# Kernel optimization log

Hardware: AMD Instinct MI355X
Metric: run time of the kernel (lower is better)

The kernel has to match this reference:

```python
import jax, jax.numpy as jnp
import numpy as np

DIM = 1024
H = 56
NS = 32            # n_state == head_v_dim
KEY_DIM = H * NS   # 1792
D_INNER = H * NS   # 1792
T_LEN = 2048
B = 4


def _xavier(key, fan_out, fan_in):
    bound = (6.0 / (fan_in + fan_out)) ** 0.5
    return jax.random.uniform(key, (fan_out, fan_in), jnp.float32, -bound, bound)


def setup_inputs() -> dict:
    key = jax.random.key(0)
    ks = jax.random.split(key, 8)
    x = jax.random.normal(ks[0], (T_LEN, B, DIM), jnp.float32)
    S = jnp.zeros((B, H, NS, NS), jnp.float32)
    Wq = _xavier(ks[1], KEY_DIM, DIM)
    Wk = _xavier(ks[2], KEY_DIM, DIM)
    Wv = _xavier(ks[3], D_INNER, DIM)
    Wa = _xavier(ks[4], H, DIM)
    Wout = _xavier(ks[5], DIM, D_INNER)
    A_log = jax.random.uniform(ks[6], (H,), jnp.float32, -5.0, -1.0)
    dt_bias = jax.random.uniform(ks[7], (H,), jnp.float32, 0.5, 1.5)
    return {"x": x, "S": S, "Wq": Wq, "Wk": Wk, "Wv": Wv, "Wa": Wa,
            "A_log": A_log, "dt_bias": dt_bias, "Wout": Wout}


def _l2norm(t):
    # matches F.normalize(dim=-1): x / max(||x||, 1e-12)
    n = jnp.sqrt(jnp.sum(t * t, axis=-1, keepdims=True))
    return t / jnp.maximum(n, 1e-12)


def reference(x, S, Wq, Wk, Wv, Wa, A_log, dt_bias, Wout):
    T, Bb, _ = x.shape
    q = jax.nn.silu(x @ Wq.T).reshape(T, Bb, H, NS)
    k = jax.nn.silu(x @ Wk.T).reshape(T, Bb, H, NS)
    v = jax.nn.silu(x @ Wv.T).reshape(T, Bb, H, NS)
    q = _l2norm(q)
    k = _l2norm(k)
    a = x @ Wa.T                                   # [T,B,H]
    dt = jax.nn.softplus(a + dt_bias)
    decay = jnp.exp(-jnp.exp(A_log) * dt)          # [T,B,H]

    def step(S_t, inp):
        k_t, v_t, q_t, d_t = inp                   # [B,H,NS], [B,H,NS], [B,H,NS], [B,H]
        retrieved = jnp.einsum('bhij,bhi->bhj', S_t, k_t)   # S^T k
        delta = v_t - retrieved
        outer = k_t[..., :, None] * delta[..., None, :]     # [B,H,NS,NS] = k ox delta
        S_t = S_t + jnp.tanh(d_t[..., None, None] * S_t + outer)
        Sq = jnp.einsum('bhij,bhi->bhj', S_t, q_t)
        return S_t, Sq

    S_new, out = jax.lax.scan(step, S, (k, v, q, decay))
    out = out.reshape(T, Bb, D_INNER) @ Wout.T     # [T,B,dim]
    return out, S_new
```

## Files before the change

kernel.cpp:

```cpp
#include <hip/hip_runtime.h>


typedef __attribute__((ext_vector_type(8))) __bf16 bf16x8;
typedef __attribute__((ext_vector_type(8))) _Float16 f16x8;
typedef __attribute__((ext_vector_type(4))) float f32x4;
typedef __attribute__((ext_vector_type(2))) float f32x2;

#define T_LEN 2048
#define BB 4
#define HH 56
#define NS 32
#define DIM 1024
#define KD 1792
#define MROWS 8192
#define CH 16
#define NCHUNK (T_LEN / CH)

#define VMCNT(N) asm volatile("s_waitcnt vmcnt(" #N ")" ::: "memory")
#define LGKM(N)  asm volatile("s_waitcnt lgkmcnt(" #N ")" ::: "memory")
#define SB       __builtin_amdgcn_sched_barrier(0)

__device__ __forceinline__ float bf2f(unsigned short u) {
    return __uint_as_float(((unsigned int)u) << 16);
}
__device__ __forceinline__ unsigned short f2bf(float f) {
    unsigned int u = __float_as_uint(f);
    u += 0x7fffu + ((u >> 16) & 1u);
    return (unsigned short)(u >> 16);
}
__device__ __forceinline__ unsigned short f2h(float f) {
    union { _Float16 h; unsigned short u; } cv;
    cv.h = (_Float16)f;
    return cv.u;
}
__device__ __forceinline__ float h2f(unsigned short u) {
    union { unsigned short u; _Float16 h; } cv;
    cv.u = u;
    return (float)cv.h;
}

__device__ __forceinline__ float tanh_fast(float x) {
    float e = __builtin_amdgcn_exp2f(x * 2.885390081777927f);
    float r = __builtin_amdgcn_rcpf(e + 1.0f);
    return fmaf(-2.0f, r, 1.0f);
}

__device__ __forceinline__ float dpp_sum16(float x) {
    int t;
    t = __builtin_amdgcn_update_dpp(0, __float_as_int(x), 0xB1, 0xf, 0xf, true);
    x += __int_as_float(t);
    t = __builtin_amdgcn_update_dpp(0, __float_as_int(x), 0x4E, 0xf, 0xf, true);
    x += __int_as_float(t);
    t = __builtin_amdgcn_update_dpp(0, __float_as_int(x), 0x141, 0xf, 0xf, true);
    x += __int_as_float(t);
    t = __builtin_amdgcn_update_dpp(0, __float_as_int(x), 0x140, 0xf, 0xf, true);
    x += __int_as_float(t);
    return x;
}

__device__ __forceinline__ f32x2 dpp_sum16x2(float a, float b) {
    int ta, tb;
    ta = __builtin_amdgcn_update_dpp(0, __float_as_int(a), 0xB1, 0xf, 0xf, true);
    tb = __builtin_amdgcn_update_dpp(0, __float_as_int(b), 0xB1, 0xf, 0xf, true);
    a += __int_as_float(ta); b += __int_as_float(tb);
    ta = __builtin_amdgcn_update_dpp(0, __float_as_int(a), 0x4E, 0xf, 0xf, true);
    tb = __builtin_amdgcn_update_dpp(0, __float_as_int(b), 0x4E, 0xf, 0xf, true);
    a += __int_as_float(ta); b += __int_as_float(tb);
    ta = __builtin_amdgcn_update_dpp(0, __float_as_int(a), 0x141, 0xf, 0xf, true);
    tb = __builtin_amdgcn_update_dpp(0, __float_as_int(b), 0x141, 0xf, 0xf, true);
    a += __int_as_float(ta); b += __int_as_float(tb);
    ta = __builtin_amdgcn_update_dpp(0, __float_as_int(a), 0x140, 0xf, 0xf, true);
    tb = __builtin_amdgcn_update_dpp(0, __float_as_int(b), 0x140, 0xf, 0xf, true);
    a += __int_as_float(ta); b += __int_as_float(tb);
    return (f32x2){a, b};
}

__device__ __forceinline__ void gload_lds16(const void* g, void* l) {
    __builtin_amdgcn_global_load_lds(
        (const __attribute__((address_space(1))) unsigned int*)g,
        (__attribute__((address_space(3))) unsigned int*)l, 16, 0, 0);
}
__device__ __forceinline__ void gload_lds4(const void* g, void* l) {
    __builtin_amdgcn_global_load_lds(
        (const __attribute__((address_space(1))) unsigned int*)g,
        (__attribute__((address_space(3))) unsigned int*)l, 4, 0, 0);
}

__device__ __forceinline__ unsigned lds_off(const void* p) {
    return (unsigned)(unsigned long long)
        (const __attribute__((address_space(3))) char*)p;
}

template <int OFF>
__device__ __forceinline__ f32x4 dsr128(unsigned a) {
    f32x4 r;
    asm volatile("ds_read_b128 %0, %1 offset:%2" : "=v"(r) : "v"(a), "n"(OFF));
    return r;
}
template <int OFF>
__device__ __forceinline__ f32x2 dsr64f(unsigned a) {
    f32x2 r;
    asm volatile("ds_read_b64 %0, %1 offset:%2" : "=v"(r) : "v"(a), "n"(OFF));
    return r;
}
template <int OFF>
__device__ __forceinline__ unsigned dsr32u(unsigned a) {
    unsigned r;
    asm volatile("ds_read_b32 %0, %1 offset:%2" : "=v"(r) : "v"(a), "n"(OFF));
    return r;
}
template <int OFF>
__device__ __forceinline__ float dsr32f(unsigned a) {
    float r;
    asm volatile("ds_read_b32 %0, %1 offset:%2" : "=v"(r) : "v"(a), "n"(OFF));
    return r;
}

__global__ void cast_split3_kernel(const float* __restrict__ in,
                                   unsigned short* __restrict__ hi,
                                   unsigned short* __restrict__ lo,
                                   unsigned short* __restrict__ h16, int n8) {
    int i = blockIdx.x * blockDim.x + threadIdx.x;
    if (i >= n8) return;
    const float4* p = (const float4*)in + (size_t)i * 2;
    float4 a = p[0], b = p[1];
    float xs[8] = {a.x, a.y, a.z, a.w, b.x, b.y, b.z, b.w};
    unsigned int ho[4], lv[4], hv[4];
#pragma unroll
    for (int c = 0; c < 4; ++c) {
        unsigned short h0 = f2bf(xs[2 * c]);
        unsigned short h1 = f2bf(xs[2 * c + 1]);
        unsigned short l0 = f2bf(xs[2 * c] - bf2f(h0));
        unsigned short l1 = f2bf(xs[2 * c + 1] - bf2f(h1));
        ho[c] = (unsigned int)h0 | ((unsigned int)h1 << 16);
        lv[c] = (unsigned int)l0 | ((unsigned int)l1 << 16);
        hv[c] = (unsigned int)f2h(xs[2 * c]) | ((unsigned int)f2h(xs[2 * c + 1]) << 16);
    }
    ((uint4*)hi)[i]  = (uint4){ho[0], ho[1], ho[2], ho[3]};
    ((uint4*)lo)[i]  = (uint4){lv[0], lv[1], lv[2], lv[3]};
    ((uint4*)h16)[i] = (uint4){hv[0], hv[1], hv[2], hv[3]};
}

__global__ void cast_split_kernel(const float* __restrict__ in,
                                  unsigned short* __restrict__ hi,
                                  unsigned short* __restrict__ lo, int n8) {
    int i = blockIdx.x * blockDim.x + threadIdx.x;
    if (i >= n8) return;
    const float4* p = (const float4*)in + (size_t)i * 2;
    float4 a = p[0], b = p[1];
    float xs[8] = {a.x, a.y, a.z, a.w, b.x, b.y, b.z, b.w};
    unsigned int ho[4], lv[4];
#pragma unroll
    for (int c = 0; c < 4; ++c) {
        unsigned short h0 = f2bf(xs[2 * c]);
        unsigned short h1 = f2bf(xs[2 * c + 1]);
        unsigned short l0 = f2bf(xs[2 * c] - bf2f(h0));
        unsigned short l1 = f2bf(xs[2 * c + 1] - bf2f(h1));
        ho[c] = (unsigned int)h0 | ((unsigned int)h1 << 16);
        lv[c] = (unsigned int)l0 | ((unsigned int)l1 << 16);
    }
    ((uint4*)hi)[i] = (uint4){ho[0], ho[1], ho[2], ho[3]};
    ((uint4*)lo)[i] = (uint4){lv[0], lv[1], lv[2], lv[3]};
}

__global__ void cast_half_kernel(const float* __restrict__ in,
                                 unsigned short* __restrict__ out, int n8) {
    int i = blockIdx.x * blockDim.x + threadIdx.x;
    if (i >= n8) return;
    const float4* p = (const float4*)in + (size_t)i * 2;
    float4 a = p[0], b = p[1];
    uint4 o;
    o.x = (unsigned int)f2h(a.x) | ((unsigned int)f2h(a.y) << 16);
    o.y = (unsigned int)f2h(a.z) | ((unsigned int)f2h(a.w) << 16);
    o.z = (unsigned int)f2h(b.x) | ((unsigned int)f2h(b.y) << 16);
    o.w = (unsigned int)f2h(b.z) | ((unsigned int)f2h(b.w) << 16);
    ((uint4*)out)[i] = o;
}

__device__ __forceinline__ void gemm_split(
    const unsigned short* __restrict__ Ah, const unsigned short* __restrict__ Al,
    const unsigned short* __restrict__ Bh, const unsigned short* __restrict__ Bl,
    int m0, int n0, int K, int bmax,
    unsigned short* AsH, unsigned short* AsL,
    unsigned short* BsH, unsigned short* BsL,
    f32x4 (&acc)[4][4]) {
    const int tid  = threadIdx.x;
    const int lane = tid & 63;
    const int wave = tid >> 6;
    const int wm = wave >> 1, wn = wave & 1;
    const int lr = lane & 15, lkb = lane >> 4;

#pragma unroll
    for (int fr = 0; fr < 4; ++fr)
#pragma unroll
        for (int fc = 0; fc < 4; ++fc) acc[fr][fc] = (f32x4){0.f, 0.f, 0.f, 0.f};

    auto stage = [&](int kt) {
#pragma unroll
        for (int c = 0; c < 2; ++c) {
            int i = c * 256 + tid;
            int r = i >> 2, kk = (i & 3) << 3;
            size_t ao = (size_t)(m0 + r) * K + kt + kk;
            int br = n0 + r; if (br > bmax) br = bmax;
            size_t bo = (size_t)br * K + kt + kk;
            gload_lds16(Ah + ao, AsH + i * 8);
            gload_lds16(Al + ao, AsL + i * 8);
            gload_lds16(Bh + bo, BsH + i * 8);
            gload_lds16(Bl + bo, BsL + i * 8);
        }
    };

    stage(0);
    const int nk = K >> 5;
    for (int t = 0; t < nk; ++t) {
        __syncthreads();
        bf16x8 ah[4], al[4], bh[4], bl[4];
#pragma unroll
        for (int f = 0; f < 4; ++f) {
            int ai = (wm * 64 + f * 16 + lr) * 32 + lkb * 8;
            int bi = (wn * 64 + f * 16 + lr) * 32 + lkb * 8;
            ah[f] = *(const bf16x8*)(AsH + ai);
            al[f] = *(const bf16x8*)(AsL + ai);
            bh[f] = *(const bf16x8*)(BsH + bi);
            bl[f] = *(const bf16x8*)(BsL + bi);
        }
#pragma unroll
        for (int fr = 0; fr < 4; ++fr)
#pragma unroll
            for (int fc = 0; fc < 4; ++fc) {
                acc[fr][fc] = __builtin_amdgcn_mfma_f32_16x16x32_bf16(
                    ah[fr], bh[fc], acc[fr][fc], 0, 0, 0);
                acc[fr][fc] = __builtin_amdgcn_mfma_f32_16x16x32_bf16(
                    ah[fr], bl[fc], acc[fr][fc], 0, 0, 0);
                acc[fr][fc] = __builtin_amdgcn_mfma_f32_16x16x32_bf16(
                    al[fr], bh[fc], acc[fr][fc], 0, 0, 0);
            }
        __syncthreads();
        if (t + 1 < nk) stage((t + 1) << 5);
    }
}

__global__ __launch_bounds__(256) void proj_split_kernel(
    const unsigned short* __restrict__ xh, const unsigned short* __restrict__ xl,
    const unsigned short* __restrict__ Wh, const unsigned short* __restrict__ Wl,
    const unsigned short* __restrict__ Wah, const unsigned short* __restrict__ Wal,
    const float* __restrict__ A_log, const float* __restrict__ dt_bias,
    float* __restrict__ dstF, float* __restrict__ decayb, int knorm) {
    __shared__ __align__(16) unsigned short AsH[128 * 32];
    __shared__ __align__(16) unsigned short AsL[128 * 32];
    __shared__ __align__(16) unsigned short BsH[128 * 32];
    __shared__ __align__(16) unsigned short BsL[128 * 32];

    const int tile = blockIdx.x;
    const bool isdecay = (tile == 14);
    int m0 = blockIdx.y * 128;
    int n0 = isdecay ? 0 : tile * 128;
    int bmax = isdecay ? (HH - 1) : (KD - 1);
    const unsigned short* Bh = isdecay ? Wah : Wh;
    const unsigned short* Bl = isdecay ? Wal : Wl;

    f32x4 acc[4][4];
    gemm_split(xh, xl, Bh, Bl, m0, n0, DIM, bmax, AsH, AsL, BsH, BsL, acc);

    const int lane = threadIdx.x & 63, wave = threadIdx.x >> 6;
    const int wm = wave >> 1, wn = wave & 1, lr = lane & 15, lkb = lane >> 4;

    if (isdecay) {
#pragma unroll
        for (int fr = 0; fr < 4; ++fr)
#pragma unroll
            for (int fc = 0; fc < 4; ++fc)
#pragma unroll
                for (int v = 0; v < 4; ++v) {
                    int m = m0 + wm * 64 + fr * 16 + lkb * 4 + v;
                    int n = n0 + wn * 64 + fc * 16 + lr;
                    int t = m >> 2, b = m & 3;
                    if (n < HH) {
                        float z = acc[fr][fc][v] + dt_bias[n];
                        float sp = (z > 20.f) ? z : log1pf(__expf(z));
                        decayb[((size_t)(b * HH + n)) * T_LEN + t] =
                            __expf(-__expf(A_log[n]) * sp);
                    }
                }
        return;
    }

    if (knorm) {
#pragma unroll
        for (int fr = 0; fr < 4; ++fr)
#pragma unroll
            for (int hc = 0; hc < 2; ++hc)
#pragma unroll
                for (int v = 0; v < 4; ++v) {
                    float yA = acc[fr][2 * hc][v];
                    float yB = acc[fr][2 * hc + 1][v];
                    float sA = yA / (1.f + __expf(-yA));
                    float sB = yB / (1.f + __expf(-yB));
                    float ss = fmaf(sA, sA, sB * sB);
                    ss = dpp_sum16(ss);
                    float sc = 1.f / fmaxf(sqrtf(ss), 1e-12f);
                    int m = m0 + wm * 64 + fr * 16 + lkb * 4 + v;
                    int t = m >> 2, b = m & 3;
                    int h = ((n0 + wn * 64) >> 5) + hc;
                    size_t ro = (((size_t)(b * HH + h)) * T_LEN + t) * NS;
                    dstF[ro + lr]      = sA * sc;
                    dstF[ro + lr + 16] = sB * sc;
                }
    } else {
#pragma unroll
        for (int fr = 0; fr < 4; ++fr)
#pragma unroll
            for (int fc = 0; fc < 4; ++fc)
#pragma unroll
                for (int v = 0; v < 4; ++v) {
                    int m = m0 + wm * 64 + fr * 16 + lkb * 4 + v;
                    int n = n0 + wn * 64 + fc * 16 + lr;
                    int t = m >> 2, b = m & 3;
                    int h = n >> 5, i = n & 31;
                    float y = acc[fr][fc][v];
                    float s = y / (1.f + __expf(-y));
                    dstF[(((size_t)(b * HH + h)) * T_LEN + t) * NS + i] = s;
                }
    }
}

__global__ __launch_bounds__(256) void q_gemm_f16_kernel(
    const unsigned short* __restrict__ xf, const unsigned short* __restrict__ Wqf,
    unsigned short* __restrict__ dstH) {
    __shared__ __align__(16) unsigned short As[128 * 32];
    __shared__ __align__(16) unsigned short Bs[128 * 32];
    int m0 = blockIdx.y * 128, n0 = blockIdx.x * 128;

    const int tid  = threadIdx.x;
    const int lane = tid & 63;
    const int wave = tid >> 6;
    const int wm = wave >> 1, wn = wave & 1;
    const int lr = lane & 15, lkb = lane >> 4;

    f32x4 acc[4][4];
#pragma unroll
    for (int fr = 0; fr < 4; ++fr)
#pragma unroll
        for (int fc = 0; fc < 4; ++fc) acc[fr][fc] = (f32x4){0.f, 0.f, 0.f, 0.f};

    auto stage = [&](int kt) {
#pragma unroll
        for (int c = 0; c < 2; ++c) {
            int i = c * 256 + tid;
            int r = i >> 2, kk = (i & 3) << 3;
            gload_lds16(xf + (size_t)(m0 + r) * DIM + kt + kk, As + i * 8);
            gload_lds16(Wqf + (size_t)(n0 + r) * DIM + kt + kk, Bs + i * 8);
        }
    };

    stage(0);
    const int nk = DIM >> 5;
    for (int t = 0; t < nk; ++t) {
        __syncthreads();
        f16x8 af[4], bf[4];
#pragma unroll
        for (int f = 0; f < 4; ++f) {
            af[f] = *(const f16x8*)(As + (wm * 64 + f * 16 + lr) * 32 + lkb * 8);
            bf[f] = *(const f16x8*)(Bs + (wn * 64 + f * 16 + lr) * 32 + lkb * 8);
        }
#pragma unroll
        for (int fr = 0; fr < 4; ++fr)
#pragma unroll
            for (int fc = 0; fc < 4; ++fc)
                acc[fr][fc] = __builtin_amdgcn_mfma_f32_16x16x32_f16(
                    af[fr], bf[fc], acc[fr][fc], 0, 0, 0);
        __syncthreads();
        if (t + 1 < nk) stage((t + 1) << 5);
    }

#pragma unroll
    for (int fr = 0; fr < 4; ++fr)
#pragma unroll
        for (int hc = 0; hc < 2; ++hc)
#pragma unroll
            for (int v = 0; v < 4; ++v) {
                float yA = acc[fr][2 * hc][v];
                float yB = acc[fr][2 * hc + 1][v];
                float sA = yA / (1.f + __expf(-yA));
                float sB = yB / (1.f + __expf(-yB));
                float ss = fmaf(sA, sA, sB * sB);
                ss = dpp_sum16(ss);
                float sc = 1.f / fmaxf(sqrtf(ss), 1e-12f);
                int m = m0 + wm * 64 + fr * 16 + lkb * 4 + v;
                int t = m >> 2, b = m & 3;
                int h = ((n0 + wn * 64) >> 5) + hc;
                size_t ro = (((size_t)(b * HH + h)) * T_LEN + t) * NS;
                dstH[ro + lr]      = f2h(sA * sc);
                dstH[ro + lr + 16] = f2h(sB * sc);
            }
}

__global__ __launch_bounds__(256) void out_gemm_kernel(
    const unsigned short* __restrict__ Sq, const unsigned short* __restrict__ Wo,
    float* __restrict__ out) {
    __shared__ __align__(16) unsigned short As[128 * 32];
    __shared__ __align__(16) unsigned short Bs[128 * 32];
    int m0 = blockIdx.y * 128, n0 = blockIdx.x * 128;

    const int tid  = threadIdx.x;
    const int lane = tid & 63;
    const int wave = tid >> 6;
    const int wm = wave >> 1, wn = wave & 1;
    const int lr = lane & 15, lkb = lane >> 4;

    f32x4 acc[4][4];
#pragma unroll
    for (int fr = 0; fr < 4; ++fr)
#pragma unroll
        for (int fc = 0; fc < 4; ++fc) acc[fr][fc] = (f32x4){0.f, 0.f, 0.f, 0.f};

    auto stage = [&](int kt) {
#pragma unroll
        for (int c = 0; c < 2; ++c) {
            int i = c * 256 + tid;
            int r = i >> 2, kk = (i & 3) << 3;
            gload_lds16(Sq + (size_t)(m0 + r) * KD + kt + kk, As + i * 8);
            gload_lds16(Wo + (size_t)(n0 + r) * KD + kt + kk, Bs + i * 8);
        }
    };

    stage(0);
    const int nk = KD >> 5;
    for (int t = 0; t < nk; ++t) {
        __syncthreads();
        f16x8 af[4], bf[4];
#pragma unroll
        for (int f = 0; f < 4; ++f) {
            af[f] = *(const f16x8*)(As + (wm * 64 + f * 16 + lr) * 32 + lkb * 8);
            bf[f] = *(const f16x8*)(Bs + (wn * 64 + f * 16 + lr) * 32 + lkb * 8);
        }
#pragma unroll
        for (int fr = 0; fr < 4; ++fr)
#pragma unroll
            for (int fc = 0; fc < 4; ++fc)
                acc[fr][fc] = __builtin_amdgcn_mfma_f32_16x16x32_f16(
                    af[fr], bf[fc], acc[fr][fc], 0, 0, 0);
        __syncthreads();
        if (t + 1 < nk) stage((t + 1) << 5);
    }

#pragma unroll
    for (int fr = 0; fr < 4; ++fr)
#pragma unroll
        for (int fc = 0; fc < 4; ++fc)
#pragma unroll
            for (int v = 0; v < 4; ++v) {
                int m = m0 + wm * 64 + fr * 16 + lkb * 4 + v;
                int n = n0 + wn * 64 + fc * 16 + lr;
                out[(size_t)m * DIM + n] = acc[fr][fc][v];
            }
}

__global__ __launch_bounds__(512, 1) void scan_kernel(
    const float* __restrict__ kf, const unsigned short* __restrict__ qh,
    const float* __restrict__ vf, const float* __restrict__ decayb,
    const float* __restrict__ S0, unsigned short* __restrict__ Sq,
    float* __restrict__ Sout) {
    __shared__ __align__(16) float          kbuf[4][CH][NS];
    __shared__ __align__(16) float          vbuf[4][CH][NS];
    __shared__ __align__(16) unsigned short qbuf[4][CH][NS];
    __shared__ __align__(16) float          dbuf[4][64];

    const int bh = blockIdx.x;
    const int b = bh / HH, h = bh - b * HH;
    const int tid = threadIdx.x;
    const int lane = tid & 63, wave = tid >> 6;
    const int col = tid >> 4;
    const int ii  = tid & 15;
    const int i0  = ii * 2;

    const float* Sp = S0 + (size_t)bh * NS * NS;
    float s0 = Sp[(i0 + 0) * NS + col];
    float s1 = Sp[(i0 + 1) * NS + col];

    const size_t base  = (size_t)bh * T_LEN * NS;
    const size_t dbase = (size_t)bh * T_LEN;
    const size_t cbcol = (size_t)h * NS;

    const unsigned kb0 = lds_off(&kbuf[0][0][0]) + (unsigned)i0 * 4;
    const unsigned qb0 = lds_off(&qbuf[0][0][0]) + (unsigned)i0 * 2;
    const unsigned vb0 = lds_off(&vbuf[0][0][0]) + (unsigned)col * 4;
    const unsigned db0 = lds_off(&dbuf[0][0]);

    auto stage = [&](int c) {
        int s = c & 3;
        if (wave == 0) {
            gload_lds16(kf + base + (size_t)c * 512 + lane * 4,
                        &kbuf[s][0][0] + lane * 4);
        } else if (wave == 1) {
            gload_lds16(kf + base + (size_t)c * 512 + 256 + lane * 4,
                        &kbuf[s][8][0] + lane * 4);
        } else if (wave == 2) {
            gload_lds16(vf + base + (size_t)c * 512 + lane * 4,
                        &vbuf[s][0][0] + lane * 4);
        } else if (wave == 3) {
            gload_lds16(vf + base + (size_t)c * 512 + 256 + lane * 4,
                        &vbuf[s][8][0] + lane * 4);
        } else if (wave == 4) {
            gload_lds16(qh + base + (size_t)c * 512 + lane * 8,
                        &qbuf[s][0][0] + lane * 8);
        } else if (wave == 5) {
            gload_lds4(decayb + dbase + (size_t)c * CH + lane,
                       &dbuf[s][0] + lane);
        }
    };

    stage(0);
    stage(1);
    VMCNT(0);
    __builtin_amdgcn_s_barrier();

    float o_pend = 0.f;

    for (int c = 0; c < NCHUNK; ++c) {
        if (c + 2 < NCHUNK) stage(c + 2);
        if (wave < 6) { VMCNT(18); }
        __builtin_amdgcn_s_barrier();
        SB;

        const int s = c & 3;
        const unsigned kb = kb0 + (unsigned)s * (CH * NS * 4);
        const unsigned qb = qb0 + (unsigned)s * (CH * NS * 2);
        const unsigned vb = vb0 + (unsigned)s * (CH * NS * 4);
        const unsigned db = db0 + (unsigned)s * 256;

        f32x2 kA[4], kB[4]; unsigned qA[4], qB[4]; float vA[4], vB[4];
        f32x4 dA, dB;

#define LDG(KK, QQ, VV, DV, g)                                          \
        KK[0] = dsr64f<((g) * 4 + 0) * 128>(kb);                        \
        KK[1] = dsr64f<((g) * 4 + 1) * 128>(kb);                        \
        KK[2] = dsr64f<((g) * 4 + 2) * 128>(kb);                        \
        KK[3] = dsr64f<((g) * 4 + 3) * 128>(kb);                        \
        QQ[0] = dsr32u<((g) * 4 + 0) * 64>(qb);                         \
        QQ[1] = dsr32u<((g) * 4 + 1) * 64>(qb);                         \
        QQ[2] = dsr32u<((g) * 4 + 2) * 64>(qb);                         \
        QQ[3] = dsr32u<((g) * 4 + 3) * 64>(qb);                         \
        VV[0] = dsr32f<((g) * 4 + 0) * 128>(vb);                        \
        VV[1] = dsr32f<((g) * 4 + 1) * 128>(vb);                        \
        VV[2] = dsr32f<((g) * 4 + 2) * 128>(vb);                        \
        VV[3] = dsr32f<((g) * 4 + 3) * 128>(vb);                        \
        DV    = dsr128<(g) * 16>(db);

#define CMP(KK, QQ, VV, DV, g)                                          \
        {                                                               \
            _Pragma("unroll")                                           \
            for (int p = 0; p < 4; ++p) {                               \
                const int t = c * CH + (g) * 4 + p;                     \
                float k0 = KK[p][0], k1 = KK[p][1];                     \
                float q0 = h2f((unsigned short)(QQ[p] & 0xffff));       \
                float q1 = h2f((unsigned short)(QQ[p] >> 16));          \
                float vj = VV[p];                                       \
                float d  = DV[p];                                       \
                float xr = fmaf(k1, s1, k0 * s0);                       \
                f32x2 rd = dpp_sum16x2(xr, o_pend);                     \
                if (ii == 0 && t > 0) {                                 \
                    size_t ro = ((size_t)(t - 1) * BB + b) * KD + cbcol;\
                    Sq[ro + col] = f2h(rd[1]);                          \
                }                                                       \
                float delta = vj - rd[0];                               \
                float a0 = fmaf(d, s0, k0 * delta);                     \
                float a1 = fmaf(d, s1, k1 * delta);                     \
                s0 += tanh_fast(a0); s1 += tanh_fast(a1);               \
                o_pend = fmaf(q1, s1, q0 * s0);                         \
            }                                                           \
        }

        LDG(kA, qA, vA, dA, 0);
        LDG(kB, qB, vB, dB, 1);
        LGKM(13); SB;
        CMP(kA, qA, vA, dA, 0);
        LDG(kA, qA, vA, dA, 2);
        LGKM(13); SB;
        CMP(kB, qB, vB, dB, 1);
        LDG(kB, qB, vB, dB, 3);
        LGKM(13); SB;
        CMP(kA, qA, vA, dA, 2);
        LGKM(0); SB;
        CMP(kB, qB, vB, dB, 3);
#undef LDG
#undef CMP
    }

    {
        float oo = dpp_sum16(o_pend);
        if (ii == 0) {
            size_t ro = ((size_t)(T_LEN - 1) * BB + b) * KD + cbcol;
            Sq[ro + col] = f2h(oo);
        }
    }

    float* so = Sout + (size_t)bh * NS * NS;
    so[(i0 + 0) * NS + col] = s0;
    so[(i0 + 1) * NS + col] = s1;
}

extern "C" void kernel_launch(void* const* d_in, const int* in_sizes, int n_in,
                              void* d_out, int out_size, void* d_ws, size_t ws_size,
                              hipStream_t stream) {
    const float* x       = (const float*)d_in[0];
    const float* S0      = (const float*)d_in[1];
    const float* Wq      = (const float*)d_in[2];
    const float* Wk      = (const float*)d_in[3];
    const float* Wv      = (const float*)d_in[4];
    const float* Wa      = (const float*)d_in[5];
    const float* A_log   = (const float*)d_in[6];
    const float* dt_bias = (const float*)d_in[7];
    const float* Wout    = (const float*)d_in[8];

    float* out  = (float*)d_out;
    float* Sout = out + (size_t)T_LEN * BB * DIM;

    char* w = (char*)d_ws;
    auto alloc = [&](size_t bytes) {
        char* p = w; w += (bytes + 255) & ~(size_t)255; return p;
    };
    unsigned short* xh  = (unsigned short*)alloc((size_t)MROWS * DIM * 2);
    unsigned short* xl  = (unsigned short*)alloc((size_t)MROWS * DIM * 2);
    unsigned short* Wbh = (unsigned short*)alloc((size_t)KD * DIM * 2);
    unsigned short* Wbl = (unsigned short*)alloc((size_t)KD * DIM * 2);
    unsigned short* Wah = (unsigned short*)alloc((size_t)HH * DIM * 2);
    unsigned short* Wal = (unsigned short*)alloc((size_t)HH * DIM * 2);
    float* kf           = (float*)alloc((size_t)MROWS * KD * 4);
    float* vf           = (float*)alloc((size_t)MROWS * KD * 4);
    unsigned short* Woh = (unsigned short*)alloc((size_t)DIM * KD * 2);
    unsigned short* Sq   = xh;
    unsigned short* xf16 = (unsigned short*)vf;

    unsigned short* qh  = (unsigned short*)d_out;
    float* decayb       = (float*)((char*)d_out + (size_t)MROWS * KD * 2);

    {
        int n8 = (int)((size_t)MROWS * DIM / 8);
        cast_split3_kernel<<<(n8 + 255) / 256, 256, 0, stream>>>(x, xh, xl, xf16, n8);
    }
    {
        int n8 = (int)((size_t)KD * DIM / 8);
        cast_half_kernel<<<(n8 + 255) / 256, 256, 0, stream>>>(Wq, Wbh, n8);
        q_gemm_f16_kernel<<<dim3(14, 64), 256, 0, stream>>>(xf16, Wbh, qh);
    }
    {
        int n8 = (int)((size_t)KD * DIM / 8);
        cast_split_kernel<<<(n8 + 255) / 256, 256, 0, stream>>>(Wk, Wbh, Wbl, n8);
        int n8a = (int)((size_t)HH * DIM / 8);
        cast_split_kernel<<<(n8a + 255) / 256, 256, 0, stream>>>(Wa, Wah, Wal, n8a);
        proj_split_kernel<<<dim3(15, 64), 256, 0, stream>>>(
            xh, xl, Wbh, Wbl, Wah, Wal, A_log, dt_bias, kf, decayb, 1);
    }
    {
        int n8 = (int)((size_t)KD * DIM / 8);
        cast_split_kernel<<<(n8 + 255) / 256, 256, 0, stream>>>(Wv, Wbh, Wbl, n8);
        proj_split_kernel<<<dim3(14, 64), 256, 0, stream>>>(
            xh, xl, Wbh, Wbl, Wah, Wal, A_log, dt_bias, vf, decayb, 0);
    }
    {
        int n8 = (int)((size_t)DIM * KD / 8);
        cast_half_kernel<<<(n8 + 255) / 256, 256, 0, stream>>>(Wout, Woh, n8);
    }
    scan_kernel<<<BB * HH, 512, 0, stream>>>(kf, qh, vf, decayb, S0, Sq, Sout);
    out_gemm_kernel<<<dim3(8, 64), 256, 0, stream>>>(Sq, Woh, out);
}
```

Baseline: 716.1 us.

## Fuse cast kernels, merge k/v projection launches, enlarge scan chunk with LDS-staged output

All fp32-to-bf16/fp16 weight and input casts now run in one kernel, which needs separate buffers for each weight. The k, v and decay projections are merged into one launch of 29 column tiles. The scan kernel doubles its chunk length to 32, unrolling more compute groups per barrier. It also buffers per-step outputs in LDS and has an idle wave write them out as coalesced 16-byte stores instead of scattered 2-byte stores. These changes cut launch count and tail effects and improve store coalescing, at the cost of more LDS and workspace plus retuned wait counts.

```diff
diff --git a/kernel.cpp b/kernel.cpp
--- a/kernel.cpp
+++ b/kernel.cpp
@@ -13,7 +13,7 @@
 #define DIM 1024
 #define KD 1792
 #define MROWS 8192
-#define CH 16
+#define CH 32
 #define NCHUNK (T_LEN / CH)
 
 #define VMCNT(N) asm volatile("s_waitcnt vmcnt(" #N ")" ::: "memory")
@@ -116,16 +116,12 @@
     return r;
 }
 
-__global__ void cast_split3_kernel(const float* __restrict__ in,
-                                   unsigned short* __restrict__ hi,
-                                   unsigned short* __restrict__ lo,
-                                   unsigned short* __restrict__ h16, int n8) {
-    int i = blockIdx.x * blockDim.x + threadIdx.x;
-    if (i >= n8) return;
+__device__ __forceinline__ void do_split8(const float* in, unsigned short* hi,
+                                          unsigned short* lo, int i) {
     const float4* p = (const float4*)in + (size_t)i * 2;
     float4 a = p[0], b = p[1];
     float xs[8] = {a.x, a.y, a.z, a.w, b.x, b.y, b.z, b.w};
-    unsigned int ho[4], lv[4], hv[4];
+    unsigned int ho[4], lv[4];
 #pragma unroll
     for (int c = 0; c < 4; ++c) {
         unsigned short h0 = f2bf(xs[2 * c]);
@@ -134,39 +130,11 @@
         unsigned short l1 = f2bf(xs[2 * c + 1] - bf2f(h1));
         ho[c] = (unsigned int)h0 | ((unsigned int)h1 << 16);
         lv[c] = (unsigned int)l0 | ((unsigned int)l1 << 16);
-        hv[c] = (unsigned int)f2h(xs[2 * c]) | ((unsigned int)f2h(xs[2 * c + 1]) << 16);
-    }
-    ((uint4*)hi)[i]  = (uint4){ho[0], ho[1], ho[2], ho[3]};
-    ((uint4*)lo)[i]  = (uint4){lv[0], lv[1], lv[2], lv[3]};
-    ((uint4*)h16)[i] = (uint4){hv[0], hv[1], hv[2], hv[3]};
-}
-
-__global__ void cast_split_kernel(const float* __restrict__ in,
-                                  unsigned short* __restrict__ hi,
-                                  unsigned short* __restrict__ lo, int n8) {
-    int i = blockIdx.x * blockDim.x + threadIdx.x;
-    if (i >= n8) return;
-    const float4* p = (const float4*)in + (size_t)i * 2;
-    float4 a = p[0], b = p[1];
-    float xs[8] = {a.x, a.y, a.z, a.w, b.x, b.y, b.z, b.w};
-    unsigned int ho[4], lv[4];
-#pragma unroll
-    for (int c = 0; c < 4; ++c) {
-        unsigned short h0 = f2bf(xs[2 * c]);
-        unsigned short h1 = f2bf(xs[2 * c + 1]);
-        unsigned short l0 = f2bf(xs[2 * c] - bf2f(h0));
-        unsigned short l1 = f2bf(xs[2 * c + 1] - bf2f(h1));
-        ho[c] = (unsigned int)h0 | ((unsigned int)h1 << 16);
-        lv[c] = (unsigned int)l0 | ((unsigned int)l1 << 16);
     }
     ((uint4*)hi)[i] = (uint4){ho[0], ho[1], ho[2], ho[3]};
     ((uint4*)lo)[i] = (uint4){lv[0], lv[1], lv[2], lv[3]};
 }
-
-__global__ void cast_half_kernel(const float* __restrict__ in,
-                                 unsigned short* __restrict__ out, int n8) {
-    int i = blockIdx.x * blockDim.x + threadIdx.x;
-    if (i >= n8) return;
+__device__ __forceinline__ void do_half8(const float* in, unsigned short* out, int i) {
     const float4* p = (const float4*)in + (size_t)i * 2;
     float4 a = p[0], b = p[1];
     uint4 o;
@@ -176,6 +144,55 @@
     o.w = (unsigned int)f2h(b.z) | ((unsigned int)f2h(b.w) << 16);
     ((uint4*)out)[i] = o;
 }
+
+__global__ void megacast_kernel(
+    const float* __restrict__ x, unsigned short* __restrict__ xh,
+    unsigned short* __restrict__ xl, unsigned short* __restrict__ xf16,
+    const float* __restrict__ Wk, unsigned short* __restrict__ Wkh,
+    unsigned short* __restrict__ Wkl,
+    const float* __restrict__ Wv, unsigned short* __restrict__ Wvh,
+    unsigned short* __restrict__ Wvl,
+    const float* __restrict__ Wa, unsigned short* __restrict__ Wah,
+    unsigned short* __restrict__ Wal,
+    const float* __restrict__ Wq, unsigned short* __restrict__ Wqh16,
+    const float* __restrict__ Wout, unsigned short* __restrict__ Woh) {
+    int i = blockIdx.x * blockDim.x + threadIdx.x;
+    const int N0 = MROWS * DIM / 8;
+    const int N1 = KD * DIM / 8;
+    const int N3 = HH * DIM / 8;
+    if (i < N0) {
+        const float4* p = (const float4*)x + (size_t)i * 2;
+        float4 a = p[0], b = p[1];
+        float xs[8] = {a.x, a.y, a.z, a.w, b.x, b.y, b.z, b.w};
+        unsigned int ho[4], lv[4], hv[4];
+#pragma unroll
+        for (int c = 0; c < 4; ++c) {
+            unsigned short h0 = f2bf(xs[2 * c]);
+            unsigned short h1 = f2bf(xs[2 * c + 1]);
+            unsigned short l0 = f2bf(xs[2 * c] - bf2f(h0));
+            unsigned short l1 = f2bf(xs[2 * c + 1] - bf2f(h1));
+            ho[c] = (unsigned int)h0 | ((unsigned int)h1 << 16);
+            lv[c] = (unsigned int)l0 | ((unsigned int)l1 << 16);
+            hv[c] = (unsigned int)f2h(xs[2 * c]) |
+                    ((unsigned int)f2h(xs[2 * c + 1]) << 16);
+        }
+        ((uint4*)xh)[i]   = (uint4){ho[0], ho[1], ho[2], ho[3]};
+        ((uint4*)xl)[i]   = (uint4){lv[0], lv[1], lv[2], lv[3]};
+        ((uint4*)xf16)[i] = (uint4){hv[0], hv[1], hv[2], hv[3]};
+        return;
+    }
+    i -= N0;
+    if (i < N1) { do_split8(Wk, Wkh, Wkl, i); return; }
+    i -= N1;
+    if (i < N1) { do_split8(Wv, Wvh, Wvl, i); return; }
+    i -= N1;
+    if (i < N3) { do_split8(Wa, Wah, Wal, i); return; }
+    i -= N3;
+    if (i < N1) { do_half8(Wq, Wqh16, i); return; }
+    i -= N1;
+    if (i < N1) { do_half8(Wout, Woh, i); }
+}
+#define MEGACAST_ITEMS (MROWS * DIM / 8 + 4 * (KD * DIM / 8) + HH * DIM / 8)
 
 __device__ __forceinline__ void gemm_split(
     const unsigned short* __restrict__ Ah, const unsigned short* __restrict__ Al,
@@ -240,24 +257,26 @@
     }
 }
 
-__global__ __launch_bounds__(256) void proj_split_kernel(
+__global__ __launch_bounds__(256) void kv_proj_kernel(
     const unsigned short* __restrict__ xh, const unsigned short* __restrict__ xl,
-    const unsigned short* __restrict__ Wh, const unsigned short* __restrict__ Wl,
+    const unsigned short* __restrict__ Wkh, const unsigned short* __restrict__ Wkl,
+    const unsigned short* __restrict__ Wvh, const unsigned short* __restrict__ Wvl,
     const unsigned short* __restrict__ Wah, const unsigned short* __restrict__ Wal,
     const float* __restrict__ A_log, const float* __restrict__ dt_bias,
-    float* __restrict__ dstF, float* __restrict__ decayb, int knorm) {
+    float* __restrict__ kf, float* __restrict__ vf,
+    float* __restrict__ decayb) {
     __shared__ __align__(16) unsigned short AsH[128 * 32];
     __shared__ __align__(16) unsigned short AsL[128 * 32];
     __shared__ __align__(16) unsigned short BsH[128 * 32];
     __shared__ __align__(16) unsigned short BsL[128 * 32];
 
     const int tile = blockIdx.x;
-    const bool isdecay = (tile == 14);
+    int mode; const unsigned short *Bh, *Bl; int n0;
+    if (tile < 14)       { mode = 0; Bh = Wkh; Bl = Wkl; n0 = tile * 128; }
+    else if (tile == 14) { mode = 1; Bh = Wah; Bl = Wal; n0 = 0; }
+    else                 { mode = 2; Bh = Wvh; Bl = Wvl; n0 = (tile - 15) * 128; }
     int m0 = blockIdx.y * 128;
-    int n0 = isdecay ? 0 : tile * 128;
-    int bmax = isdecay ? (HH - 1) : (KD - 1);
-    const unsigned short* Bh = isdecay ? Wah : Wh;
-    const unsigned short* Bl = isdecay ? Wal : Wl;
+    int bmax = (mode == 1) ? (HH - 1) : (KD - 1);
 
     f32x4 acc[4][4];
     gemm_split(xh, xl, Bh, Bl, m0, n0, DIM, bmax, AsH, AsL, BsH, BsL, acc);
@@ -265,7 +284,7 @@
     const int lane = threadIdx.x & 63, wave = threadIdx.x >> 6;
     const int wm = wave >> 1, wn = wave & 1, lr = lane & 15, lkb = lane >> 4;
 
-    if (isdecay) {
+    if (mode == 1) {
 #pragma unroll
         for (int fr = 0; fr < 4; ++fr)
 #pragma unroll
@@ -285,7 +304,7 @@
         return;
     }
 
-    if (knorm) {
+    if (mode == 0) {
 #pragma unroll
         for (int fr = 0; fr < 4; ++fr)
 #pragma unroll
@@ -303,8 +322,8 @@
                     int t = m >> 2, b = m & 3;
                     int h = ((n0 + wn * 64) >> 5) + hc;
                     size_t ro = (((size_t)(b * HH + h)) * T_LEN + t) * NS;
-                    dstF[ro + lr]      = sA * sc;
-                    dstF[ro + lr + 16] = sB * sc;
+                    kf[ro + lr]      = sA * sc;
+                    kf[ro + lr + 16] = sB * sc;
                 }
     } else {
 #pragma unroll
@@ -319,7 +338,7 @@
                     int h = n >> 5, i = n & 31;
                     float y = acc[fr][fc][v];
                     float s = y / (1.f + __expf(-y));
-                    dstF[(((size_t)(b * HH + h)) * T_LEN + t) * NS + i] = s;
+                    vf[(((size_t)(b * HH + h)) * T_LEN + t) * NS + i] = s;
                 }
     }
 }
@@ -465,6 +484,7 @@
     __shared__ __align__(16) float          vbuf[4][CH][NS];
     __shared__ __align__(16) unsigned short qbuf[4][CH][NS];
     __shared__ __align__(16) float          dbuf[4][64];
+    __shared__ __align__(16) unsigned short obuf[4][CH][NS];
 
     const int bh = blockIdx.x;
     const int b = bh / HH, h = bh - b * HH;
@@ -490,23 +510,39 @@
     auto stage = [&](int c) {
         int s = c & 3;
         if (wave == 0) {
-            gload_lds16(kf + base + (size_t)c * 512 + lane * 4,
-                        &kbuf[s][0][0] + lane * 4);
+            const float* src = kf + base + (size_t)c * (CH * NS);
+            gload_lds16(src + lane * 4,       &kbuf[s][0][0] + lane * 4);
+            gload_lds16(src + 256 + lane * 4, &kbuf[s][8][0] + lane * 4);
         } else if (wave == 1) {
-            gload_lds16(kf + base + (size_t)c * 512 + 256 + lane * 4,
-                        &kbuf[s][8][0] + lane * 4);
+            const float* src = kf + base + (size_t)c * (CH * NS);
+            gload_lds16(src + 512 + lane * 4, &kbuf[s][16][0] + lane * 4);
+            gload_lds16(src + 768 + lane * 4, &kbuf[s][24][0] + lane * 4);
         } else if (wave == 2) {
-            gload_lds16(vf + base + (size_t)c * 512 + lane * 4,
-                        &vbuf[s][0][0] + lane * 4);
+            const float* src = vf + base + (size_t)c * (CH * NS);
+            gload_lds16(src + lane * 4,       &vbuf[s][0][0] + lane * 4);
+            gload_lds16(src + 256 + lane * 4, &vbuf[s][8][0] + lane * 4);
         } else if (wave == 3) {
-            gload_lds16(vf + base + (size_t)c * 512 + 256 + lane * 4,
-                        &vbuf[s][8][0] + lane * 4);
+            const float* src = vf + base + (size_t)c * (CH * NS);
+            gload_lds16(src + 512 + lane * 4, &vbuf[s][16][0] + lane * 4);
+            gload_lds16(src + 768 + lane * 4, &vbuf[s][24][0] + lane * 4);
         } else if (wave == 4) {
-            gload_lds16(qh + base + (size_t)c * 512 + lane * 8,
-                        &qbuf[s][0][0] + lane * 8);
+            const unsigned short* src = qh + base + (size_t)c * (CH * NS);
+            gload_lds16(src + lane * 8,       &qbuf[s][0][0] + lane * 8);
+            gload_lds16(src + 512 + lane * 8, &qbuf[s][16][0] + lane * 8);
         } else if (wave == 5) {
             gload_lds4(decayb + dbase + (size_t)c * CH + lane,
                        &dbuf[s][0] + lane);
+        }
+    };
+
+    auto flush = [&](int cc) {
+#pragma unroll
+        for (int kk = 0; kk < 2; ++kk) {
+            int row = kk * 16 + (lane >> 2);
+            int seg = (lane & 3) * 8;
+            uint4 dv = *(const uint4*)(&obuf[cc & 3][row][seg]);
+            size_t go = ((size_t)(cc * CH + row) * BB + b) * KD + cbcol + seg;
+            *(uint4*)(Sq + go) = dv;
         }
     };
 
@@ -519,9 +555,10 @@
 
     for (int c = 0; c < NCHUNK; ++c) {
         if (c + 2 < NCHUNK) stage(c + 2);
-        if (wave < 6) { VMCNT(18); }
+        if (wave < 6) { VMCNT(4); }
         __builtin_amdgcn_s_barrier();
         SB;
+        if (wave == 6 && c >= 2) flush(c - 2);
 
         const int s = c & 3;
         const unsigned kb = kb0 + (unsigned)s * (CH * NS * 4);
@@ -551,7 +588,6 @@
         {                                                               \
             _Pragma("unroll")                                           \
             for (int p = 0; p < 4; ++p) {                               \
-                const int t = c * CH + (g) * 4 + p;                     \
                 float k0 = KK[p][0], k1 = KK[p][1];                     \
                 float q0 = h2f((unsigned short)(QQ[p] & 0xffff));       \
                 float q1 = h2f((unsigned short)(QQ[p] >> 16));          \
@@ -559,9 +595,12 @@
                 float d  = DV[p];                                       \
                 float xr = fmaf(k1, s1, k0 * s0);                       \
                 f32x2 rd = dpp_sum16x2(xr, o_pend);                     \
-                if (ii == 0 && t > 0) {                                 \
-                    size_t ro = ((size_t)(t - 1) * BB + b) * KD + cbcol;\
-                    Sq[ro + col] = f2h(rd[1]);                          \
+                if (ii == 0) {                                          \
+                    if ((g) == 0 && p == 0) {                           \
+                        if (c > 0) obuf[(c + 3) & 3][CH - 1][col] = f2h(rd[1]); \
+                    } else {                                            \
+                        obuf[s][(g) * 4 + p - 1][col] = f2h(rd[1]);     \
+                    }                                                   \
                 }                                                       \
                 float delta = vj - rd[0];                               \
                 float a0 = fmaf(d, s0, k0 * delta);                     \
@@ -581,19 +620,30 @@
         LDG(kB, qB, vB, dB, 3);
         LGKM(13); SB;
         CMP(kA, qA, vA, dA, 2);
+        LDG(kA, qA, vA, dA, 4);
+        LGKM(13); SB;
+        CMP(kB, qB, vB, dB, 3);
+        LDG(kB, qB, vB, dB, 5);
+        LGKM(13); SB;
+        CMP(kA, qA, vA, dA, 4);
+        LDG(kA, qA, vA, dA, 6);
+        LGKM(13); SB;
+        CMP(kB, qB, vB, dB, 5);
+        LDG(kB, qB, vB, dB, 7);
+        LGKM(13); SB;
+        CMP(kA, qA, vA, dA, 6);
         LGKM(0); SB;
-        CMP(kB, qB, vB, dB, 3);
+        CMP(kB, qB, vB, dB, 7);
 #undef LDG
 #undef CMP
     }
 
     {
         float oo = dpp_sum16(o_pend);
-        if (ii == 0) {
-            size_t ro = ((size_t)(T_LEN - 1) * BB + b) * KD + cbcol;
-            Sq[ro + col] = f2h(oo);
-        }
-    }
+        if (ii == 0) obuf[(NCHUNK - 1) & 3][CH - 1][col] = f2h(oo);
+    }
+    __builtin_amdgcn_s_barrier();
+    if (wave == 6) { flush(NCHUNK - 2); flush(NCHUNK - 1); }
 
     float* so = Sout + (size_t)bh * NS * NS;
     so[(i0 + 0) * NS + col] = s0;
@@ -620,15 +670,18 @@
     auto alloc = [&](size_t bytes) {
         char* p = w; w += (bytes + 255) & ~(size_t)255; return p;
     };
-    unsigned short* xh  = (unsigned short*)alloc((size_t)MROWS * DIM * 2);
-    unsigned short* xl  = (unsigned short*)alloc((size_t)MROWS * DIM * 2);
-    unsigned short* Wbh = (unsigned short*)alloc((size_t)KD * DIM * 2);
-    unsigned short* Wbl = (unsigned short*)alloc((size_t)KD * DIM * 2);
-    unsigned short* Wah = (unsigned short*)alloc((size_t)HH * DIM * 2);
-    unsigned short* Wal = (unsigned short*)alloc((size_t)HH * DIM * 2);
-    float* kf           = (float*)alloc((size_t)MROWS * KD * 4);
-    float* vf           = (float*)alloc((size_t)MROWS * KD * 4);
-    unsigned short* Woh = (unsigned short*)alloc((size_t)DIM * KD * 2);
+    unsigned short* xh    = (unsigned short*)alloc((size_t)MROWS * DIM * 2);
+    unsigned short* xl    = (unsigned short*)alloc((size_t)MROWS * DIM * 2);
+    unsigned short* Wkh   = (unsigned short*)alloc((size_t)KD * DIM * 2);
+    unsigned short* Wkl   = (unsigned short*)alloc((size_t)KD * DIM * 2);
+    unsigned short* Wvh   = (unsigned short*)alloc((size_t)KD * DIM * 2);
+    unsigned short* Wvl   = (unsigned short*)alloc((size_t)KD * DIM * 2);
+    unsigned short* Wah   = (unsigned short*)alloc((size_t)HH * DIM * 2);
+    unsigned short* Wal   = (unsigned short*)alloc((size_t)HH * DIM * 2);
+    unsigned short* Wqh16 = (unsigned short*)alloc((size_t)KD * DIM * 2);
+    float* kf             = (float*)alloc((size_t)MROWS * KD * 4);
+    float* vf             = (float*)alloc((size_t)MROWS * KD * 4);
+    unsigned short* Woh   = (unsigned short*)alloc((size_t)DIM * KD * 2);
     unsigned short* Sq   = xh;
     unsigned short* xf16 = (unsigned short*)vf;
 
@@ -636,32 +689,14 @@
     float* decayb       = (float*)((char*)d_out + (size_t)MROWS * KD * 2);
 
     {
-        int n8 = (int)((size_t)MROWS * DIM / 8);
-        cast_split3_kernel<<<(n8 + 255) / 256, 256, 0, stream>>>(x, xh, xl, xf16, n8);
-    }
-    {
-        int n8 = (int)((size_t)KD * DIM / 8);
-        cast_half_kernel<<<(n8 + 255) / 256, 256, 0, stream>>>(Wq, Wbh, n8);
-        q_gemm_f16_kernel<<<dim3(14, 64), 256, 0, stream>>>(xf16, Wbh, qh);
-    }
-    {
-        int n8 = (int)((size_t)KD * DIM / 8);
-        cast_split_kernel<<<(n8 + 255) / 256, 256, 0, stream>>>(Wk, Wbh, Wbl, n8);
-        int n8a = (int)((size_t)HH * DIM / 8);
-        cast_split_kernel<<<(n8a + 255) / 256, 256, 0, stream>>>(Wa, Wah, Wal, n8a);
-        proj_split_kernel<<<dim3(15, 64), 256, 0, stream>>>(
-            xh, xl, Wbh, Wbl, Wah, Wal, A_log, dt_bias, kf, decayb, 1);
-    }
-    {
-        int n8 = (int)((size_t)KD * DIM / 8);
-        cast_split_kernel<<<(n8 + 255) / 256, 256, 0, stream>>>(Wv, Wbh, Wbl, n8);
-        proj_split_kernel<<<dim3(14, 64), 256, 0, stream>>>(
-            xh, xl, Wbh, Wbl, Wah, Wal, A_log, dt_bias, vf, decayb, 0);
-    }
-    {
-        int n8 = (int)((size_t)DIM * KD / 8);
-        cast_half_kernel<<<(n8 + 255) / 256, 256, 0, stream>>>(Wout, Woh, n8);
-    }
+        int items = MEGACAST_ITEMS;
+        megacast_kernel<<<(items + 255) / 256, 256, 0, stream>>>(
+            x, xh, xl, xf16, Wk, Wkh, Wkl, Wv, Wvh, Wvl,
+            Wa, Wah, Wal, Wq, Wqh16, Wout, Woh);
+    }
+    q_gemm_f16_kernel<<<dim3(14, 64), 256, 0, stream>>>(xf16, Wqh16, qh);
+    kv_proj_kernel<<<dim3(29, 64), 256, 0, stream>>>(
+        xh, xl, Wkh, Wkl, Wvh, Wvl, Wah, Wal, A_log, dt_bias, kf, vf, decayb);
     scan_kernel<<<BB * HH, 512, 0, stream>>>(kf, qh, vf, decayb, S0, Sq, Sout);
     out_gemm_kernel<<<dim3(8, 64), 256, 0, stream>>>(Sq, Woh, out);
 }
```

Result: faster. 663.3 us (-7.4%).
